# Kernel tuning notes

Measured on AMD Instinct MI355X. Metric: run time of the kernel, lower is better.

The kernel has to match this reference:

```python
import jax, jax.numpy as jnp
import numpy as np

EMBED_DIM = 1024
N_HEAD = 16
HEAD_DIM = EMBED_DIM // N_HEAD


def setup_inputs() -> dict:
    key = jax.random.key(0)
    k1, k2, k3 = jax.random.split(key, 3)
    B, S = 2, 2048
    x = jax.random.normal(k1, (B, S, EMBED_DIM), dtype=jnp.float32)
    # kaiming-style scale for the packed QKV projection and output projection
    w_qkv = jax.random.normal(k2, (3 * EMBED_DIM, EMBED_DIM), dtype=jnp.float32) * np.sqrt(2.0 / EMBED_DIM)
    w0 = jax.random.normal(k3, (EMBED_DIM, EMBED_DIM), dtype=jnp.float32) * np.sqrt(2.0 / EMBED_DIM)
    return {"x": x, "w_qkv": w_qkv, "w0": w0}


def reference(x, w_qkv, w0):
    B, S, E = x.shape
    # fused QKV projection (Linear with no bias): x @ w_qkv.T -> [B,S,3E]
    qkv = jnp.einsum('bse,fe->bsf', x, w_qkv)
    q, k, v = jnp.split(qkv, 3, axis=-1)
    # reshape to [B, H, S, D]
    def heads(t):
        return t.reshape(B, S, N_HEAD, HEAD_DIM).transpose(0, 2, 1, 3)
    q, k, v = heads(q), heads(k), heads(v)
    scale = 1.0 / np.sqrt(HEAD_DIM).astype(np.float32)
    scores = jnp.einsum('bhsd,bhtd->bhst', q, k) * scale  # [B,H,S,S]
    # causal additive bias: -inf above the diagonal (same math as the precomputed bias tensor)
    causal = jnp.tril(jnp.ones((S, S), dtype=bool))
    scores = jnp.where(causal, scores, -jnp.inf)
    probs = jax.nn.softmax(scores, axis=-1)
    e = jnp.einsum('bhst,bhtd->bhsd', probs, v)  # [B,H,S,D]
    e = e.transpose(0, 2, 1, 3).reshape(B, S, E)
    # output projection: E @ w0.T
    return jnp.einsum('bse,fe->bsf', e, w0)
```

## Files before the change

### kernel.cpp

```cpp
#include <hip/hip_runtime.h>


typedef unsigned short u16;
typedef short bf16x8 __attribute__((ext_vector_type(8)));
typedef float f32x4 __attribute__((ext_vector_type(4)));
typedef unsigned short u16x4 __attribute__((ext_vector_type(4)));

#define S_LEN 2048
#define EMB 1024
#define NH 16
#define HD 64
#define QKV_W 3072
#define BATCH 2
#define CSC 0.18033688f
#define PSTR 72

static __device__ __forceinline__ u16 f2bf(float f) {
    unsigned x = __float_as_uint(f);
    return (u16)((x + 0x7fffu + ((x >> 16) & 1u)) >> 16);
}

static __device__ __forceinline__ void gld_lds16(const u16* g, u16* l) {
    __builtin_amdgcn_global_load_lds(
        (const __attribute__((address_space(1))) void*)g,
        (__attribute__((address_space(3))) void*)l, 16, 0, 0);
}

#define XN4 (BATCH * S_LEN * EMB / 4)
#define WQ4 (QKV_W * EMB / 4)
#define W04 (EMB * EMB / 4)
__global__ __launch_bounds__(256) void cvt_all(const float* __restrict__ x,
                                               const float* __restrict__ wq,
                                               const float* __restrict__ w0,
                                               u16* __restrict__ xb,
                                               u16* __restrict__ wqb,
                                               u16* __restrict__ w0b) {
    int i = blockIdx.x * 256 + threadIdx.x;
    const float* src;
    u16* dst;
    int off;
    if (i < XN4) { src = x; dst = xb; off = i; }
    else if (i < XN4 + WQ4) { src = wq; dst = wqb; off = i - XN4; }
    else { src = w0; dst = w0b; off = i - XN4 - WQ4; }
    float4 v = ((const float4*)src)[off];
    u16x4 o;
    o[0] = f2bf(v.x); o[1] = f2bf(v.y); o[2] = f2bf(v.z); o[3] = f2bf(v.w);
    ((u16x4*)dst)[off] = o;
}

template <typename OutT, int BN>
__global__ __launch_bounds__(256) void gemm_bt(const u16* __restrict__ A,
                                               const u16* __restrict__ Bt,
                                               OutT* __restrict__ C,
                                               int M, int N, int K, int qcols) {
    constexpr int NF = BN / 32;
    __shared__ alignas(16) u16 As[128 * 32];
    __shared__ alignas(16) u16 Bs[BN * 32];
    const int tid = threadIdx.x;
    const int wave = tid >> 6, lane = tid & 63;
    const int quad = lane >> 4, lr = lane & 15;
    const int m0 = blockIdx.y * 128, n0 = blockIdx.x * BN;
    const int wm = (wave & 1) * 64, wn = (wave >> 1) * (BN / 2);
    const float sc = (n0 < qcols) ? CSC : 1.0f;

    f32x4 acc[4][NF] = {};

    for (int k0 = 0; k0 < K; k0 += 32) {
#pragma unroll
        for (int i = 0; i < 2; ++i) {
            int chunk = tid + i * 256;
            int row = chunk >> 2;
            int col8 = (chunk & 3) * 8;
            gld_lds16(&A[(size_t)(m0 + row) * K + k0 + col8], &As[row * 32 + col8]);
        }
#pragma unroll
        for (int i = 0; i < BN / 64; ++i) {
            int chunk = tid + i * 256;
            int row = chunk >> 2;
            int col8 = (chunk & 3) * 8;
            gld_lds16(&Bt[(size_t)(n0 + row) * K + k0 + col8], &Bs[row * 32 + col8]);
        }
        __syncthreads();
        bf16x8 af[4], bf[NF];
#pragma unroll
        for (int i = 0; i < 4; ++i)
            af[i] = *(const bf16x8*)&As[(wm + i * 16 + lr) * 32 + quad * 8];
#pragma unroll
        for (int i = 0; i < NF; ++i)
            bf[i] = *(const bf16x8*)&Bs[(wn + i * 16 + lr) * 32 + quad * 8];
#pragma unroll
        for (int mi = 0; mi < 4; ++mi)
#pragma unroll
            for (int ni = 0; ni < NF; ++ni)
                acc[mi][ni] = __builtin_amdgcn_mfma_f32_16x16x32_bf16(
                    af[mi], bf[ni], acc[mi][ni], 0, 0, 0);
        __syncthreads();
    }

#pragma unroll
    for (int mi = 0; mi < 4; ++mi) {
#pragma unroll
        for (int r = 0; r < 4; ++r) {
            int gr = m0 + wm + mi * 16 + quad * 4 + r;
#pragma unroll
            for (int ni = 0; ni < NF; ++ni) {
                int gc = n0 + wn + ni * 16 + lr;
                float v = acc[mi][ni][r] * sc;
                if constexpr (sizeof(OutT) == 2)
                    C[(size_t)gr * N + gc] = (OutT)f2bf(v);
                else
                    C[(size_t)gr * N + gc] = (OutT)v;
            }
        }
    }
}

__global__ __launch_bounds__(256) void transpose_v(const u16* __restrict__ qkv,
                                                   u16* __restrict__ vt) {
    __shared__ alignas(16) u16 t[64][72];
    const int s0 = blockIdx.x * 64;
    const int bh = blockIdx.y;
    const int b = bh >> 4, h = bh & 15;
#pragma unroll
    for (int i = 0; i < 2; ++i) {
        int chunk = threadIdx.x + i * 256;
        int row = chunk >> 3;
        int c8 = (chunk & 7) * 8;
        uint4 v = *(const uint4*)&qkv[(size_t)(b * S_LEN + s0 + row) * QKV_W +
                                      2 * EMB + h * HD + c8];
        const u16* p = (const u16*)&v;
#pragma unroll
        for (int jj = 0; jj < 8; ++jj) t[c8 + jj][row] = p[jj];
    }
    __syncthreads();
#pragma unroll
    for (int i = 0; i < 2; ++i) {
        int chunk = threadIdx.x + i * 256;
        int d = chunk >> 3;
        int c8 = (chunk & 7) * 8;
        uint4 v = *(const uint4*)&t[d][c8];
        *(uint4*)&vt[((size_t)bh * HD + d) * S_LEN + s0 + c8] = v;
    }
}

__global__ __launch_bounds__(512, 4) void attn(const u16* __restrict__ qkv,
                                               const u16* __restrict__ vt,
                                               u16* __restrict__ e) {
    const int tid = threadIdx.x;
    const int w = tid >> 6, lane = tid & 63;
    const int quad = lane >> 4, lr = lane & 15;
    const int wq = w & 3, hv = w >> 2;
    const int tA = blockIdx.x;
    const int tB = 31 - tA;
    const int bh = blockIdx.y, b = bh >> 4, h = bh & 15;

    __shared__ alignas(16) u16 smem[25600];
    u16* Ks = smem;
    u16* Vs = smem + 8192;
    u16* pw = smem + 16384 + w * 16 * PSTR;

    const u16* qkv_b = qkv + (size_t)b * S_LEN * QKV_W;
    const u16* qrowA = qkv_b + (size_t)(tA * 64 + wq * 16 + lr) * QKV_W + h * HD + quad * 8;
    const u16* qrowB = qkv_b + (size_t)(tB * 64 + wq * 16 + lr) * QKV_W + h * HD + quad * 8;
    const bf16x8 qfA0 = *(const bf16x8*)(qrowA);
    const bf16x8 qfA1 = *(const bf16x8*)(qrowA + 32);
    const bf16x8 qfB0 = *(const bf16x8*)(qrowB);
    const bf16x8 qfB1 = *(const bf16x8*)(qrowB + 32);

    const u16* kbase = qkv_b + EMB + h * HD;
    const u16* vbase = vt + (size_t)bh * HD * S_LEN;

    f32x4 oA[4] = {}, oB[4] = {};
    float lsA = 0.f, lsB = 0.f;
    const int qgA = tA * 64 + wq * 16 + lr;
    const int qgB = tB * 64 + wq * 16 + lr;

    const int sr = wq * 16 + (lane >> 2);
    const int scl = (lane & 3) * 8;
    const int scg = ((lane & 3) ^ ((lane >> 3) & 3)) * 8;

    auto stage = [&](int j, int bb) {
        const int kv0 = j * 64;
        if (w < 4) {
            gld_lds16(kbase + (size_t)(kv0 + sr) * QKV_W + scg,
                      &Ks[bb * 4096 + sr * 32 + scl]);
            gld_lds16(kbase + (size_t)(kv0 + sr) * QKV_W + 32 + scg,
                      &Ks[bb * 4096 + 2048 + sr * 32 + scl]);
        } else {
            gld_lds16(vbase + (size_t)sr * S_LEN + kv0 + scg,
                      &Vs[bb * 4096 + sr * 32 + scl]);
            gld_lds16(vbase + (size_t)sr * S_LEN + kv0 + 32 + scg,
                      &Vs[bb * 4096 + 2048 + sr * 32 + scl]);
        }
    };

    const int xq8 = (quad ^ ((lr >> 1) & 3)) * 8;

    stage(0, 0);
    for (int j = 0; j <= tB; ++j) {
        const int bb = j & 1;
        __syncthreads();
        if (j < tB) stage(j + 1, 1 - bb);
        const bool doA = (j <= tA);
        const u16* ks = &Ks[bb * 4096];
        const u16* vs = &Vs[bb * 4096];
        const int kvh = hv * 32;

        f32x4 sB[2], sA[2];
#pragma unroll
        for (int nt = 0; nt < 2; ++nt) {
            const int kvr = kvh + nt * 16 + lr;
            bf16x8 k0 = *(const bf16x8*)&ks[kvr * 32 + xq8];
            bf16x8 k1 = *(const bf16x8*)&ks[2048 + kvr * 32 + xq8];
            f32x4 z = {};
            z = __builtin_amdgcn_mfma_f32_16x16x32_bf16(k0, qfB0, z, 0, 0, 0);
            z = __builtin_amdgcn_mfma_f32_16x16x32_bf16(k1, qfB1, z, 0, 0, 0);
            sB[nt] = z;
            if (doA) {
                f32x4 za = {};
                za = __builtin_amdgcn_mfma_f32_16x16x32_bf16(k0, qfA0, za, 0, 0, 0);
                za = __builtin_amdgcn_mfma_f32_16x16x32_bf16(k1, qfA1, za, 0, 0, 0);
                sA[nt] = za;
            }
        }

        const int kvg = j * 64 + kvh;
        __builtin_amdgcn_wave_barrier();
#pragma unroll
        for (int nt = 0; nt < 2; ++nt) {
            float p[4];
#pragma unroll
            for (int r = 0; r < 4; ++r) {
                float pv = exp2f(sB[nt][r]);
                if (j == tB) pv = (kvg + nt * 16 + quad * 4 + r > qgB) ? 0.f : pv;
                p[r] = pv;
            }
            lsB += (p[0] + p[1]) + (p[2] + p[3]);
            uint2 pk;
            pk.x = __builtin_amdgcn_perm(__float_as_uint(p[1]),
                                         __float_as_uint(p[0]), 0x07060302u);
            pk.y = __builtin_amdgcn_perm(__float_as_uint(p[3]),
                                         __float_as_uint(p[2]), 0x07060302u);
            *(uint2*)&pw[lr * PSTR + nt * 16 + quad * 4] = pk;
        }
        if (doA) {
#pragma unroll
            for (int nt = 0; nt < 2; ++nt) {
                float p[4];
#pragma unroll
                for (int r = 0; r < 4; ++r) {
                    float pv = exp2f(sA[nt][r]);
                    if (j == tA) pv = (kvg + nt * 16 + quad * 4 + r > qgA) ? 0.f : pv;
                    p[r] = pv;
                }
                lsA += (p[0] + p[1]) + (p[2] + p[3]);
                uint2 pk;
                pk.x = __builtin_amdgcn_perm(__float_as_uint(p[1]),
                                             __float_as_uint(p[0]), 0x07060302u);
                pk.y = __builtin_amdgcn_perm(__float_as_uint(p[3]),
                                             __float_as_uint(p[2]), 0x07060302u);
                *(uint2*)&pw[lr * PSTR + 32 + nt * 16 + quad * 4] = pk;
            }
        }
        __builtin_amdgcn_wave_barrier();
        const bf16x8 pB = *(const bf16x8*)&pw[lr * PSTR + quad * 8];
        bf16x8 pA = {};
        if (doA) pA = *(const bf16x8*)&pw[lr * PSTR + 32 + quad * 8];

#pragma unroll
        for (int nt = 0; nt < 4; ++nt) {
            bf16x8 v = *(const bf16x8*)&vs[hv * 2048 + (nt * 16 + lr) * 32 + xq8];
            oB[nt] = __builtin_amdgcn_mfma_f32_16x16x32_bf16(pB, v, oB[nt], 0, 0, 0);
            if (doA) oA[nt] = __builtin_amdgcn_mfma_f32_16x16x32_bf16(pA, v, oA[nt], 0, 0, 0);
        }
    }

    float lfA = lsA + __shfl_xor(lsA, 16, 64);
    lfA += __shfl_xor(lfA, 32, 64);
    float lfB = lsB + __shfl_xor(lsB, 16, 64);
    lfB += __shfl_xor(lfB, 32, 64);
    __syncthreads();
    float* mA = (float*)smem;
    float* mB = mA + 64 * 66;
    float* lAr = mB + 64 * 66;
    float* lBr = lAr + 64;
    if (hv) {
#pragma unroll
        for (int nt = 0; nt < 4; ++nt)
#pragma unroll
            for (int r = 0; r < 4; ++r)
                mA[(wq * 16 + quad * 4 + r) * 66 + nt * 16 + lr] = oA[nt][r];
        if (lane < 16) lAr[wq * 16 + lane] = lfA;
    } else {
#pragma unroll
        for (int nt = 0; nt < 4; ++nt)
#pragma unroll
            for (int r = 0; r < 4; ++r)
                mB[(wq * 16 + quad * 4 + r) * 66 + nt * 16 + lr] = oB[nt][r];
        if (lane < 16) lBr[wq * 16 + lane] = lfB;
    }
    __syncthreads();
    if (!hv) {
        float lff = lfA + lAr[wq * 16 + lr];
#pragma unroll
        for (int r = 0; r < 4; ++r) {
            float inv = 1.0f / __shfl(lff, quad * 4 + r, 64);
            size_t row = (size_t)(b * S_LEN + tA * 64 + wq * 16 + quad * 4 + r) * EMB + h * HD;
#pragma unroll
            for (int nt = 0; nt < 4; ++nt)
                e[row + nt * 16 + lr] =
                    f2bf((oA[nt][r] + mA[(wq * 16 + quad * 4 + r) * 66 + nt * 16 + lr]) * inv);
        }
    } else {
        float lff = lfB + lBr[wq * 16 + lr];
#pragma unroll
        for (int r = 0; r < 4; ++r) {
            float inv = 1.0f / __shfl(lff, quad * 4 + r, 64);
            size_t row = (size_t)(b * S_LEN + tB * 64 + wq * 16 + quad * 4 + r) * EMB + h * HD;
#pragma unroll
            for (int nt = 0; nt < 4; ++nt)
                e[row + nt * 16 + lr] =
                    f2bf((oB[nt][r] + mB[(wq * 16 + quad * 4 + r) * 66 + nt * 16 + lr]) * inv);
        }
    }
}

extern "C" void kernel_launch(void* const* d_in, const int* in_sizes, int n_in,
                              void* d_out, int out_size, void* d_ws, size_t ws_size,
                              hipStream_t stream) {
    const float* x = (const float*)d_in[0];
    const float* w_qkv = (const float*)d_in[1];
    const float* w0 = (const float*)d_in[2];
    float* out = (float*)d_out;

    const size_t M = (size_t)BATCH * S_LEN;
    u16* xb = (u16*)d_ws;
    u16* wqb = xb + M * EMB;
    u16* w0b = wqb + (size_t)QKV_W * EMB;
    u16* qkvb = w0b + (size_t)EMB * EMB;
    u16* vtb = qkvb + M * QKV_W;
    u16* eb = vtb + (size_t)BATCH * NH * HD * S_LEN;

    cvt_all<<<(XN4 + WQ4 + W04) / 256, 256, 0, stream>>>(x, w_qkv, w0, xb, wqb, w0b);

    gemm_bt<u16, 128><<<dim3(QKV_W / 128, M / 128), 256, 0, stream>>>(
        xb, wqb, qkvb, (int)M, QKV_W, EMB, EMB);

    transpose_v<<<dim3(S_LEN / 64, BATCH * NH), 256, 0, stream>>>(qkvb, vtb);

    attn<<<dim3(16, BATCH * NH), 512, 0, stream>>>(qkvb, vtb, eb);

    gemm_bt<float, 64><<<dim3(EMB / 64, M / 128), 256, 0, stream>>>(
        eb, w0b, out, (int)M, EMB, EMB, 0);
}
```

Measured before the change: 183.3 us.

## Repack softmax probabilities in registers with permlane swaps instead of LDS

The attention kernel no longer writes the bf16 probability tile to a per-wave LDS scratch and reads it back in MFMA operand layout. It builds the operand directly in registers using v_permlane32_swap and v_permlane16_swap, which removes the LDS round trip and the wave barriers and shrinks shared memory so more blocks can fit per CU. The grid axes are also swapped so consecutive blocks walk over batch-heads rather than query tiles, which changes dispatch order and cache locality. The correctness of the register transposition depends on how the permlane swap lanes map, and that mapping is not checked here.

After: 183.7 us. No clear change (+0.2%).

```diff
diff --git a/kernel.cpp b/kernel.cpp
--- a/kernel.cpp
+++ b/kernel.cpp
@@ -13,7 +13,6 @@
 #define QKV_W 3072
 #define BATCH 2
 #define CSC 0.18033688f
-#define PSTR 72
 
 static __device__ __forceinline__ u16 f2bf(float f) {
     unsigned x = __float_as_uint(f);
@@ -150,14 +149,13 @@
     const int w = tid >> 6, lane = tid & 63;
     const int quad = lane >> 4, lr = lane & 15;
     const int wq = w & 3, hv = w >> 2;
-    const int tA = blockIdx.x;
+    const int tA = blockIdx.y;
     const int tB = 31 - tA;
-    const int bh = blockIdx.y, b = bh >> 4, h = bh & 15;
-
-    __shared__ alignas(16) u16 smem[25600];
+    const int bh = blockIdx.x, b = bh >> 4, h = bh & 15;
+
+    __shared__ alignas(16) u16 smem[17408];
     u16* Ks = smem;
     u16* Vs = smem + 8192;
-    u16* pw = smem + 16384 + w * 16 * PSTR;
 
     const u16* qkv_b = qkv + (size_t)b * S_LEN * QKV_W;
     const u16* qrowA = qkv_b + (size_t)(tA * 64 + wq * 16 + lr) * QKV_W + h * HD + quad * 8;
@@ -195,6 +193,35 @@
     };
 
     const int xq8 = (quad ^ ((lr >> 1) & 3)) * 8;
+
+    auto softpack = [&](const f32x4* s, bool diag, int qg, int kvg,
+                        float& lsum) -> bf16x8 {
+        float p[8];
+#pragma unroll
+        for (int nt = 0; nt < 2; ++nt)
+#pragma unroll
+            for (int r = 0; r < 4; ++r) {
+                float pv = exp2f(s[nt][r]);
+                if (diag) pv = (kvg + nt * 16 + quad * 4 + r > qg) ? 0.f : pv;
+                p[nt * 4 + r] = pv;
+            }
+        lsum += ((p[0] + p[1]) + (p[2] + p[3])) + ((p[4] + p[5]) + (p[6] + p[7]));
+        unsigned x0 = __builtin_amdgcn_perm(__float_as_uint(p[1]),
+                                            __float_as_uint(p[0]), 0x07060302u);
+        unsigned x1 = __builtin_amdgcn_perm(__float_as_uint(p[3]),
+                                            __float_as_uint(p[2]), 0x07060302u);
+        unsigned x2 = __builtin_amdgcn_perm(__float_as_uint(p[5]),
+                                            __float_as_uint(p[4]), 0x07060302u);
+        unsigned x3 = __builtin_amdgcn_perm(__float_as_uint(p[7]),
+                                            __float_as_uint(p[6]), 0x07060302u);
+        asm("v_permlane32_swap_b32 %0, %1" : "+v"(x0), "+v"(x2));
+        asm("v_permlane16_swap_b32 %0, %1" : "+v"(x0), "+v"(x2));
+        asm("v_permlane32_swap_b32 %0, %1" : "+v"(x1), "+v"(x3));
+        asm("v_permlane16_swap_b32 %0, %1" : "+v"(x1), "+v"(x3));
+        union { unsigned u[4]; bf16x8 v; } r;
+        r.u[0] = x0; r.u[1] = x1; r.u[2] = x2; r.u[3] = x3;
+        return r.v;
+    };
 
     stage(0, 0);
     for (int j = 0; j <= tB; ++j) {
@@ -225,47 +252,9 @@
         }
 
         const int kvg = j * 64 + kvh;
-        __builtin_amdgcn_wave_barrier();
-#pragma unroll
-        for (int nt = 0; nt < 2; ++nt) {
-            float p[4];
-#pragma unroll
-            for (int r = 0; r < 4; ++r) {
-                float pv = exp2f(sB[nt][r]);
-                if (j == tB) pv = (kvg + nt * 16 + quad * 4 + r > qgB) ? 0.f : pv;
-                p[r] = pv;
-            }
-            lsB += (p[0] + p[1]) + (p[2] + p[3]);
-            uint2 pk;
-            pk.x = __builtin_amdgcn_perm(__float_as_uint(p[1]),
-                                         __float_as_uint(p[0]), 0x07060302u);
-            pk.y = __builtin_amdgcn_perm(__float_as_uint(p[3]),
-                                         __float_as_uint(p[2]), 0x07060302u);
-            *(uint2*)&pw[lr * PSTR + nt * 16 + quad * 4] = pk;
-        }
-        if (doA) {
-#pragma unroll
-            for (int nt = 0; nt < 2; ++nt) {
-                float p[4];
-#pragma unroll
-                for (int r = 0; r < 4; ++r) {
-                    float pv = exp2f(sA[nt][r]);
-                    if (j == tA) pv = (kvg + nt * 16 + quad * 4 + r > qgA) ? 0.f : pv;
-                    p[r] = pv;
-                }
-                lsA += (p[0] + p[1]) + (p[2] + p[3]);
-                uint2 pk;
-                pk.x = __builtin_amdgcn_perm(__float_as_uint(p[1]),
-                                             __float_as_uint(p[0]), 0x07060302u);
-                pk.y = __builtin_amdgcn_perm(__float_as_uint(p[3]),
-                                             __float_as_uint(p[2]), 0x07060302u);
-                *(uint2*)&pw[lr * PSTR + 32 + nt * 16 + quad * 4] = pk;
-            }
-        }
-        __builtin_amdgcn_wave_barrier();
-        const bf16x8 pB = *(const bf16x8*)&pw[lr * PSTR + quad * 8];
+        const bf16x8 pB = softpack(sB, j == tB, qgB, kvg, lsB);
         bf16x8 pA = {};
-        if (doA) pA = *(const bf16x8*)&pw[lr * PSTR + 32 + quad * 8];
+        if (doA) pA = softpack(sA, j == tA, qgA, kvg, lsA);
 
 #pragma unroll
         for (int nt = 0; nt < 4; ++nt) {
@@ -348,7 +337,7 @@
 
     transpose_v<<<dim3(S_LEN / 64, BATCH * NH), 256, 0, stream>>>(qkvb, vtb);
 
-    attn<<<dim3(16, BATCH * NH), 512, 0, stream>>>(qkvb, vtb, eb);
+    attn<<<dim3(BATCH * NH, 16), 512, 0, stream>>>(qkvb, vtb, eb);
 
     gemm_bt<float, 64><<<dim3(EMB / 64, M / 128), 256, 0, stream>>>(
         eb, w0b, out, (int)M, EMB, EMB, 0);
```
